# Kernel optimization log

Hardware: AMD Instinct MI355X
Metric: run time of the kernel (lower is better)

## Reference

```python
import jax, jax.numpy as jnp
import numpy as np

GAMMA = 1.0
BIG = 1e10  # finite stand-in for +inf so gradients stay nan-free


def setup_inputs() -> dict:
    key = jax.random.key(0)
    k1, k2 = jax.random.split(key)
    input_signals = jax.random.normal(k1, (16, 1024), dtype=jnp.float32)  # B x N (equal-length signals)
    ref_signal = jax.random.normal(k2, (1024,), dtype=jnp.float32)        # M
    return {"input_signals": input_signals, "ref_signal": ref_signal}


def _softmin3(a, b, c, gamma):
    z = -jnp.stack([a, b, c], axis=0) / gamma
    return -gamma * jax.nn.logsumexp(z, axis=0)


def _sdtw(D, gamma):
    """Soft-DTW forward DP via anti-diagonal wavefront.
    D: [B, N, M] pairwise squared distances.
    Returns score [B] and padded score matrix R [B, N+1, M+1].
    """
    B, N, M = D.shape
    i_arr = jnp.arange(N + 1)
    # diagonal d holds cells (i, j=d-i); store as vector over i of length N+1
    r0 = jnp.full((B, N + 1), BIG, dtype=D.dtype).at[:, 0].set(0.0)  # d=0: R[0,0]=0
    r1 = jnp.full((B, N + 1), BIG, dtype=D.dtype)                    # d=1: borders = inf

    def shift(x):  # x[:, i] -> x[:, i-1]
        return jnp.concatenate([jnp.full((B, 1), BIG, dtype=x.dtype), x[:, :-1]], axis=1)

    def step(carry, d):
        r_dm2, r_dm1 = carry
        j_arr = d - i_arr
        valid = (i_arr >= 1) & (i_arr <= N) & (j_arr >= 1) & (j_arr <= M)
        i_safe = jnp.clip(i_arr - 1, 0, N - 1)
        j_safe = jnp.clip(j_arr - 1, 0, M - 1)
        Dd = D[:, i_safe, j_safe]  # [B, N+1], D[i-1, j-1] (0-based) = cost at cell (i,j)
        sm = _softmin3(shift(r_dm2), shift(r_dm1), r_dm1, gamma)  # diag, up, left
        rd = jnp.where(valid[None, :], Dd + sm, BIG)
        return (r_dm1, rd), rd

    ds = jnp.arange(2, N + M + 1)
    _, diags = jax.lax.scan(step, (r0, r1), ds)  # [N+M-1, B, N+1]
    full = jnp.concatenate([r0[None], r1[None], diags], axis=0)  # [N+M+1, B, N+1]
    ii, jj = jnp.meshgrid(jnp.arange(N + 1), jnp.arange(M + 1), indexing="ij")
    R = jnp.moveaxis(full[ii + jj, :, ii], -1, 0)  # [B, N+1, M+1]
    score = R[:, N, M]
    return score, R


def reference(input_signals, ref_signal):
    gamma = GAMMA
    # squared-difference cost matrix, B x N x M
    D = (input_signals[:, :, None] - ref_signal[None, None, :]) ** 2
    score, R = _sdtw(D, gamma)
    # gradient matrix E = d(score)/d(D), the soft-DTW alignment matrix
    _, vjp_fn = jax.vjp(lambda Dm: _sdtw(Dm, gamma)[0], D)
    (E,) = vjp_fn(jnp.ones_like(score))
    return score, D, R, E
```

## Files before the change

### kernel.cpp

```cpp
#include <hip/hip_runtime.h>

#define NN 1024
#define MM 1024
#define NB 16
#define BIGF 1.0e10f
#define TP 17
#define NW 8
#define OFS 5
#define CW 16
#define NA 68
#define NGI (OFS * (NW - 1) + NA)

typedef float f32x4 __attribute__((ext_vector_type(4)));

__device__ __forceinline__ float softmin3f(float a, float b, float c) {
  const float mn = fminf(a, fminf(b, c));
  const float mx = fmaxf(a, fmaxf(b, c));
  const float md = __builtin_amdgcn_fmed3f(a, b, c);
  const float s = 1.0f + __expf(mn - md) + __expf(mn - mx);
  return mn - __logf(s);
}

__global__ __launch_bounds__(256) void d_init_kernel(const float* __restrict__ x,
                                                     const float* __restrict__ y,
                                                     float* __restrict__ D) {
  size_t idx = ((size_t)blockIdx.x * blockDim.x + threadIdx.x) * 4;
  int j = (int)(idx & (MM - 1));
  size_t bi = idx >> 10;
  float xi = x[bi];
  const float4 yv = *reinterpret_cast<const float4*>(y + j);
  float t0 = xi - yv.x, t1 = xi - yv.y, t2 = xi - yv.z, t3 = xi - yv.w;
  float4 o;
  o.x = t0 * t0; o.y = t1 * t1; o.z = t2 * t2; o.w = t3 * t3;
  *reinterpret_cast<float4*>(D + idx) = o;
}

__global__ __launch_bounds__(1024) void r_bound_kernel(float* __restrict__ R) {
  int b = blockIdx.x, t = threadIdx.x;
  float* Rb = R + (size_t)b * (NN + 1) * (MM + 1);
  Rb[t + 1] = BIGF;
  Rb[(size_t)(t + 1) * (MM + 1)] = BIGF;
  if (t == 0) Rb[0] = 0.0f;
}

__global__ __launch_bounds__(512) void sdtw_fwd(const float* __restrict__ x,
                                                const float* __restrict__ y,
                                                float* __restrict__ R,
                                                float* __restrict__ score) {
  __shared__ float ypad[1152];
  __shared__ float tile[NW][2112];
  __shared__ float ringR[NW][128];
  const int b = blockIdx.x, t = threadIdx.x;
  const int w = t >> 6, l = t & 63;
  float* __restrict__ Rb = R + (size_t)b * (NN + 1) * (MM + 1);
  for (int k = t; k < 1152; k += 512)
    ypad[k] = (k >= 64 && k < 64 + MM) ? y[k - 64] : 0.0f;
  const int i1 = 128 * w + 2 * l + 1;
  const float x1 = x[b * NN + i1 - 1];
  const float x2 = x[b * NN + i1];
  float* tl = &tile[w][33 * l];
  const int wm1 = (w > 0) ? (w - 1) : 0;
  const bool L0 = (l == 0), W0 = (w == 0);
  const bool pub = (l == 63) && (w < NW - 1);
  float c1 = BIGF, c2 = BIGF, m1 = BIGF, m2 = BIGF, ringPrev = BIGF;
  __syncthreads();
  for (int G = 0; G < NGI; ++G) {
    const int a = G - OFS * w;
    if (a >= 0 && a < NA) {
      const int s0 = a * CW;
#pragma unroll 4
      for (int p = 0; p < CW; ++p) {
        const int s = s0 + p;
        const int j = s - l;
        const bool act = (j >= 1) && (j <= MM);
        float up = __shfl_up(m1, 1);
        float dg = __shfl_up(m2, 1);
        const float rc = ringR[wm1][j & 127];
        if (L0) {
          up = W0 ? BIGF : rc;
          dg = W0 ? ((j == 1) ? 0.0f : BIGF) : ringPrev;
        }
        ringPrev = act ? rc : ringPrev;
        const float yv = ypad[j + 63];
        float dv1 = x1 - yv; dv1 *= dv1;
        const float r1 = dv1 + softmin3f(dg, up, c1);
        float dv2 = x2 - yv; dv2 *= dv2;
        const float r2 = dv2 + softmin3f(c1, r1, c2);
        tl[p] = r1;
        tl[16 + p] = r2;
        if (pub && act) ringR[w][j & 127] = r2;
        m2 = act ? m1 : m2;
        m1 = act ? r2 : m1;
        c1 = act ? r1 : c1;
        c2 = act ? r2 : c2;
      }
      __builtin_amdgcn_wave_barrier();
#pragma unroll
      for (int g = 0; g < 32; ++g) {
        const int rr = 4 * g + (l >> 4);
        const int sl = l & 15;
        const int col = s0 + sl - (rr >> 1);
        const float v = tile[w][rr * 16 + (rr >> 1) + sl];
        if (col >= 1 && col <= MM)
          Rb[(size_t)(128 * w + 1 + rr) * (MM + 1) + col] = v;
      }
    }
    __syncthreads();
  }
  if (w == NW - 1 && l == 63) score[b] = m1;
}

__global__ __launch_bounds__(1024) void sdtw_bwd(const float* __restrict__ x,
                                                 const float* __restrict__ y,
                                                 const float* __restrict__ R,
                                                 float* __restrict__ E) {
  __shared__ float ypad[3088];
  __shared__ float rbx[4][NN + 2];
  __shared__ float ebx[4][NN + 2];
  __shared__ float tile[NN][TP];
  const int b = blockIdx.x, t = threadIdx.x;
  const int i = t + 1;
  const float* __restrict__ Rb = R + (size_t)b * (NN + 1) * (MM + 1);
  float* __restrict__ Eb = E + (size_t)b * (size_t)NN * MM;
  for (int k = t; k < 3088; k += 1024)
    ypad[k] = (k >= 1025 && k < 1025 + MM) ? y[k - 1025] : 0.0f;
#pragma unroll
  for (int q = 0; q < 4; ++q) { rbx[q][i] = -BIGF; ebx[q][i] = 0.0f; }
  if (t == NN - 1) {
#pragma unroll
    for (int q = 0; q < 4; ++q) { rbx[q][NN + 1] = -BIGF; ebx[q][NN + 1] = 0.0f; }
  }
  const float xi = x[b * NN + t];
  const float xi1 = x[b * NN + ((t + 1 < NN) ? (t + 1) : t)];
  const bool seedrow = (i == NN);
  float rt_e = 0.0f, rt_r = -BIGF;
  float dgn_e = 0.0f, dgn_r = -BIGF;
#pragma unroll
  for (int pass = 0; pass < 4; ++pass) {
    const int row = (pass << 8) + (t >> 2);
    const int ir = row + 1;
    const int c4 = (t & 3) << 2;
    const int jb2 = (128 << 4) - ir + c4;
    if (jb2 >= 1 && jb2 + 3 <= MM) {
      const float4 v = *reinterpret_cast<const float4*>(Rb + (size_t)ir * (MM + 1) + jb2);
      tile[row][c4] = v.x; tile[row][c4 + 1] = v.y;
      tile[row][c4 + 2] = v.z; tile[row][c4 + 3] = v.w;
    } else {
#pragma unroll
      for (int c = 0; c < 4; ++c) {
        const int jc = jb2 + c;
        tile[row][c4 + c] =
            (jc >= 1 && jc <= MM) ? Rb[(size_t)ir * (MM + 1) + jc] : -BIGF;
      }
    }
  }
  __syncthreads();
  float yj = ypad[3088 - i];

  for (int K = 128; K >= 0; --K) {
    const int d0 = K << 4;
#pragma unroll
    for (int p = 0; p < 16; ++p) {
      const int s = 15 - p;
      const int d = d0 + s;
      const int j = d - i;
      const bool act = (j >= 1) && (j <= MM);
      const float dn_r = rbx[(s + 1) & 3][i + 1];
      const float dn_e = ebx[(s + 1) & 3][i + 1];
      const float yjm1 = ypad[j + 1024];
      const float rij = tile[t][s];
      float d1 = xi1 - yjm1; d1 *= d1;
      float d2 = xi - yj;    d2 *= d2;
      float d3 = xi1 - yj;   d3 *= d3;
      const float a1 = dn_r - rij - d1;
      const float a2 = rt_r - rij - d2;
      const float a3 = dgn_r - rij - d3;
      float acc = dn_e * __expf(a1) + rt_e * __expf(a2) + dgn_e * __expf(a3);
      if (seedrow && j == MM) acc += 1.0f;
      rbx[s & 3][i] = act ? rij : -BIGF;
      ebx[s & 3][i] = act ? acc : 0.0f;
      tile[t][s] = act ? acc : 0.0f;
      rt_e = act ? acc : 0.0f;
      rt_r = act ? rij : -BIGF;
      dgn_e = dn_e; dgn_r = dn_r;
      yj = yjm1;
      __syncthreads();
    }
#pragma unroll
    for (int pass = 0; pass < 4; ++pass) {
      const int row = (pass << 8) + (t >> 2);
      const int ir = row + 1;
      const int c4 = (t & 3) << 2;
      const int jb2 = d0 - ir + c4;
      float fv[4];
#pragma unroll
      for (int c = 0; c < 4; ++c) fv[c] = tile[row][c4 + c];
      if (jb2 >= 1 && jb2 + 3 <= MM) {
        f32x4 v;
        v[0] = fv[0]; v[1] = fv[1]; v[2] = fv[2]; v[3] = fv[3];
        const float* pp = Eb + (size_t)row * MM + (jb2 - 1);
        asm volatile("global_store_dwordx4 %0, %1, off" ::"v"(pp), "v"(v) : "memory");
      } else if (jb2 + 3 >= 1 && jb2 <= MM) {
#pragma unroll
        for (int c = 0; c < 4; ++c) {
          const int jc = jb2 + c;
          if (jc >= 1 && jc <= MM) Eb[(size_t)row * MM + (jc - 1)] = fv[c];
        }
      }
      const int jn = jb2 - 16;
      if (jn >= 1 && jn + 3 <= MM) {
        const float4 v = *reinterpret_cast<const float4*>(Rb + (size_t)ir * (MM + 1) + jn);
        tile[row][c4] = v.x; tile[row][c4 + 1] = v.y;
        tile[row][c4 + 2] = v.z; tile[row][c4 + 3] = v.w;
      } else {
#pragma unroll
        for (int c = 0; c < 4; ++c) {
          const int jc = jn + c;
          tile[row][c4 + c] =
              (jc >= 1 && jc <= MM) ? Rb[(size_t)ir * (MM + 1) + jc] : -BIGF;
        }
      }
    }
    __syncthreads();
  }
}

extern "C" void kernel_launch(void* const* d_in, const int* in_sizes, int n_in,
                              void* d_out, int out_size, void* d_ws, size_t ws_size,
                              hipStream_t stream) {
  const float* x = (const float*)d_in[0];
  const float* y = (const float*)d_in[1];
  float* out = (float*)d_out;
  float* score = out;
  float* D = out + NB;
  float* R = D + (size_t)NB * NN * MM;
  float* E = R + (size_t)NB * (NN + 1) * (MM + 1);

  hipLaunchKernelGGL(d_init_kernel, dim3((NB * NN * MM) / (256 * 4)), dim3(256), 0, stream,
                     x, y, D);
  hipLaunchKernelGGL(r_bound_kernel, dim3(NB), dim3(1024), 0, stream, R);
  hipLaunchKernelGGL(sdtw_fwd, dim3(NB), dim3(512), 0, stream, x, y, R, score);
  hipLaunchKernelGGL(sdtw_bwd, dim3(NB), dim3(1024), 0, stream, x, y, R, E);
}
```

Measured before the change: 1.411 ms.

## Process two rows per thread in backward soft-DTW wavefront with 512 threads

The backward kernel now runs 512 threads, each handling two adjacent rows (odd and even tiles), in place of 1024 threads with one row each. The second row's dependency is passed in registers within the thread, and only the boundary values go through a double-buffered LDS exchange. This halves the wavefronts taking part in each per-diagonal __syncthreads and cuts LDS traffic per step. In exchange each thread does twice the serial exp work per step, which lengthens the critical path of each step.

```diff
diff --git a/kernel.cpp b/kernel.cpp
--- a/kernel.cpp
+++ b/kernel.cpp
@@ -110,91 +110,109 @@
   if (w == NW - 1 && l == 63) score[b] = m1;
 }
 
-__global__ __launch_bounds__(1024) void sdtw_bwd(const float* __restrict__ x,
-                                                 const float* __restrict__ y,
-                                                 const float* __restrict__ R,
-                                                 float* __restrict__ E) {
+__global__ __launch_bounds__(512) void sdtw_bwd(const float* __restrict__ x,
+                                                const float* __restrict__ y,
+                                                const float* __restrict__ R,
+                                                float* __restrict__ E) {
   __shared__ float ypad[3088];
-  __shared__ float rbx[4][NN + 2];
-  __shared__ float ebx[4][NN + 2];
-  __shared__ float tile[NN][TP];
+  __shared__ float tE[512][TP];
+  __shared__ float tO[512][TP];
+  __shared__ float eex[2][513];
+  __shared__ float rex[2][513];
   const int b = blockIdx.x, t = threadIdx.x;
-  const int i = t + 1;
   const float* __restrict__ Rb = R + (size_t)b * (NN + 1) * (MM + 1);
   float* __restrict__ Eb = E + (size_t)b * (size_t)NN * MM;
-  for (int k = t; k < 3088; k += 1024)
+  for (int k = t; k < 3088; k += 512)
     ypad[k] = (k >= 1025 && k < 1025 + MM) ? y[k - 1025] : 0.0f;
-#pragma unroll
-  for (int q = 0; q < 4; ++q) { rbx[q][i] = -BIGF; ebx[q][i] = 0.0f; }
-  if (t == NN - 1) {
-#pragma unroll
-    for (int q = 0; q < 4; ++q) { rbx[q][NN + 1] = -BIGF; ebx[q][NN + 1] = 0.0f; }
-  }
-  const float xi = x[b * NN + t];
-  const float xi1 = x[b * NN + ((t + 1 < NN) ? (t + 1) : t)];
-  const bool seedrow = (i == NN);
-  float rt_e = 0.0f, rt_r = -BIGF;
-  float dgn_e = 0.0f, dgn_r = -BIGF;
-#pragma unroll
-  for (int pass = 0; pass < 4; ++pass) {
-    const int row = (pass << 8) + (t >> 2);
-    const int ir = row + 1;
-    const int c4 = (t & 3) << 2;
-    const int jb2 = (128 << 4) - ir + c4;
-    if (jb2 >= 1 && jb2 + 3 <= MM) {
-      const float4 v = *reinterpret_cast<const float4*>(Rb + (size_t)ir * (MM + 1) + jb2);
-      tile[row][c4] = v.x; tile[row][c4 + 1] = v.y;
-      tile[row][c4 + 2] = v.z; tile[row][c4 + 3] = v.w;
-    } else {
-#pragma unroll
-      for (int c = 0; c < 4; ++c) {
-        const int jc = jb2 + c;
-        tile[row][c4 + c] =
-            (jc >= 1 && jc <= MM) ? Rb[(size_t)ir * (MM + 1) + jc] : -BIGF;
-      }
-    }
-  }
+  for (int k = t; k < 513; k += 512) {
+    eex[0][k] = 0.0f; eex[1][k] = 0.0f;
+    rex[0][k] = -BIGF; rex[1][k] = -BIGF;
+  }
+  const int i1 = 2 * t + 1, i2 = 2 * t + 2;
+  const float xa = x[b * NN + 2 * t];
+  const float xb = x[b * NN + 2 * t + 1];
+  const float xc = x[b * NN + min(NN - 1, 2 * t + 2)];
+  const bool seedthr = (t == 511);
+  float pE1 = 0.f, pR1 = -BIGF;
+  float pE2 = 0.f, pR2 = -BIGF;
+  float gE1 = 0.f, gR1 = -BIGF;
+  float gE2 = 0.f, gR2 = -BIGF;
+
+#define COOP_LOAD(D0N)                                                         \
+  {                                                                            \
+    _Pragma("unroll")                                                          \
+    for (int pass = 0; pass < 8; ++pass) {                                     \
+      const int row = (pass << 7) + (t >> 2);                                  \
+      const int ir = row + 1;                                                  \
+      const int c4 = (t & 3) << 2;                                             \
+      const int jn = (D0N)-ir + c4;                                            \
+      float* tp = (row & 1) ? &tO[row >> 1][0] : &tE[row >> 1][0];             \
+      if (jn >= 1 && jn + 3 <= MM) {                                           \
+        const float4 v =                                                       \
+            *reinterpret_cast<const float4*>(Rb + (size_t)ir * (MM + 1) + jn); \
+        tp[c4] = v.x; tp[c4 + 1] = v.y; tp[c4 + 2] = v.z; tp[c4 + 3] = v.w;    \
+      } else {                                                                 \
+        _Pragma("unroll")                                                      \
+        for (int c = 0; c < 4; ++c) {                                          \
+          const int jc = jn + c;                                               \
+          tp[c4 + c] =                                                         \
+              (jc >= 1 && jc <= MM) ? Rb[(size_t)ir * (MM + 1) + jc] : -BIGF;  \
+        }                                                                      \
+      }                                                                        \
+    }                                                                          \
+  }
+
+  COOP_LOAD(128 << 4)
   __syncthreads();
-  float yj = ypad[3088 - i];
 
   for (int K = 128; K >= 0; --K) {
     const int d0 = K << 4;
+    float ya = ypad[d0 + 15 - i1 + 1025];
+    float yb = ypad[d0 + 15 - i1 + 1024];
 #pragma unroll
     for (int p = 0; p < 16; ++p) {
       const int s = 15 - p;
       const int d = d0 + s;
-      const int j = d - i;
-      const bool act = (j >= 1) && (j <= MM);
-      const float dn_r = rbx[(s + 1) & 3][i + 1];
-      const float dn_e = ebx[(s + 1) & 3][i + 1];
-      const float yjm1 = ypad[j + 1024];
-      const float rij = tile[t][s];
-      float d1 = xi1 - yjm1; d1 *= d1;
-      float d2 = xi - yj;    d2 *= d2;
-      float d3 = xi1 - yj;   d3 *= d3;
-      const float a1 = dn_r - rij - d1;
-      const float a2 = rt_r - rij - d2;
-      const float a3 = dgn_r - rij - d3;
-      float acc = dn_e * __expf(a1) + rt_e * __expf(a2) + dgn_e * __expf(a3);
-      if (seedrow && j == MM) acc += 1.0f;
-      rbx[s & 3][i] = act ? rij : -BIGF;
-      ebx[s & 3][i] = act ? acc : 0.0f;
-      tile[t][s] = act ? acc : 0.0f;
-      rt_e = act ? acc : 0.0f;
-      rt_r = act ? rij : -BIGF;
-      dgn_e = dn_e; dgn_r = dn_r;
-      yj = yjm1;
+      const int j1 = d - i1;
+      const int rp = (d & 1) ^ 1, wp = d & 1;
+      const float yc = ypad[j1 + 1023];
+      const float nE = eex[rp][t + 1];
+      const float nR = rex[rp][t + 1];
+      const float r1v = tE[t][s];
+      const float r2v = tO[t][s];
+      float A = xc - yc; A *= A;
+      float B = xb - yb; B *= B;
+      float C = xc - yb; C *= C;
+      float F = xa - ya; F *= F;
+      float G = xb - ya; G *= G;
+      float e2 = nE * __expf(nR - r2v - A) + pE2 * __expf(pR2 - r2v - B) +
+                 gE2 * __expf(gR2 - r2v - C);
+      if (seedthr && d == 2048) e2 += 1.0f;
+      float e1 = pE2 * __expf(pR2 - r1v - B) + pE1 * __expf(pR1 - r1v - F) +
+                 gE1 * __expf(gR1 - r1v - G);
+      tE[t][s] = e1;
+      tO[t][s] = e2;
+      const bool act1 = (j1 >= 1) && (j1 <= MM);
+      const bool act2 = (j1 >= 2) && (j1 <= MM + 1);
+      eex[wp][t] = act1 ? e1 : 0.0f;
+      rex[wp][t] = act1 ? r1v : -BIGF;
+      gE2 = nE; gR2 = nR;
+      gE1 = pE2; gR1 = pR2;
+      pE2 = act2 ? e2 : 0.0f; pR2 = act2 ? r2v : -BIGF;
+      pE1 = act1 ? e1 : 0.0f; pR1 = act1 ? r1v : -BIGF;
+      ya = yb; yb = yc;
       __syncthreads();
     }
 #pragma unroll
-    for (int pass = 0; pass < 4; ++pass) {
-      const int row = (pass << 8) + (t >> 2);
+    for (int pass = 0; pass < 8; ++pass) {
+      const int row = (pass << 7) + (t >> 2);
       const int ir = row + 1;
       const int c4 = (t & 3) << 2;
       const int jb2 = d0 - ir + c4;
+      float* tp = (row & 1) ? &tO[row >> 1][0] : &tE[row >> 1][0];
       float fv[4];
 #pragma unroll
-      for (int c = 0; c < 4; ++c) fv[c] = tile[row][c4 + c];
+      for (int c = 0; c < 4; ++c) fv[c] = tp[c4 + c];
       if (jb2 >= 1 && jb2 + 3 <= MM) {
         f32x4 v;
         v[0] = fv[0]; v[1] = fv[1]; v[2] = fv[2]; v[3] = fv[3];
@@ -210,19 +228,18 @@
       const int jn = jb2 - 16;
       if (jn >= 1 && jn + 3 <= MM) {
         const float4 v = *reinterpret_cast<const float4*>(Rb + (size_t)ir * (MM + 1) + jn);
-        tile[row][c4] = v.x; tile[row][c4 + 1] = v.y;
-        tile[row][c4 + 2] = v.z; tile[row][c4 + 3] = v.w;
+        tp[c4] = v.x; tp[c4 + 1] = v.y; tp[c4 + 2] = v.z; tp[c4 + 3] = v.w;
       } else {
 #pragma unroll
         for (int c = 0; c < 4; ++c) {
           const int jc = jn + c;
-          tile[row][c4 + c] =
-              (jc >= 1 && jc <= MM) ? Rb[(size_t)ir * (MM + 1) + jc] : -BIGF;
+          tp[c4 + c] = (jc >= 1 && jc <= MM) ? Rb[(size_t)ir * (MM + 1) + jc] : -BIGF;
         }
       }
     }
     __syncthreads();
   }
+#undef COOP_LOAD
 }
 
 extern "C" void kernel_launch(void* const* d_in, const int* in_sizes, int n_in,
@@ -240,5 +257,5 @@
                      x, y, D);
   hipLaunchKernelGGL(r_bound_kernel, dim3(NB), dim3(1024), 0, stream, R);
   hipLaunchKernelGGL(sdtw_fwd, dim3(NB), dim3(512), 0, stream, x, y, R, score);
-  hipLaunchKernelGGL(sdtw_bwd, dim3(NB), dim3(1024), 0, stream, x, y, R, E);
-}
+  hipLaunchKernelGGL(sdtw_bwd, dim3(NB), dim3(512), 0, stream, x, y, R, E);
+}
```

Measured after the change: 1.526 ms. +8.1%, slower.
